# Optimization experiments

Measured on AMD Instinct MI355X. Metric: run time of the kernel, lower is better.

The kernel has to match this reference:

```python
import jax, jax.numpy as jnp
from jax import lax
import numpy as np

H = 512
W = 512
SIGMA = 0.1
IN_CH = [3, 66, 64, 64, 32, 32, 32, 16, 16]
OUT_CH = [64, 64, 64, 32, 32, 32, 16, 16, 16]
N_LAYERS = 9


def setup_inputs() -> dict:
    key = jax.random.key(0)
    ks = jax.random.split(key, 32)
    inp = {}
    inp['x'] = jax.random.uniform(ks[0], (3, 3, 1, 1), jnp.float32)  # query + 2 neighbor coords
    inp['neighbors'] = jax.random.uniform(ks[1], (2, 3, H, W), jnp.float32)
    inp['albedo_index'] = 4
    for i in range(N_LAYERS):
        kh = 1 if i == 0 else 3
        fan_in = IN_CH[i] * kh * kh
        inp[f'w{i}'] = jax.random.normal(ks[2 + i], (OUT_CH[i], IN_CH[i], kh, kh), jnp.float32) / np.sqrt(fan_in).astype(np.float32)
        inp[f'b{i}'] = jnp.zeros((OUT_CH[i],), jnp.float32)
    inp['wf'] = jax.random.normal(ks[20], (6, 16, 3, 3), jnp.float32) / np.sqrt(16 * 9).astype(np.float32)
    inp['bf'] = jnp.zeros((6,), jnp.float32)
    inp['albedos'] = 0.5 + jax.random.uniform(ks[21], (9, 3, H, W), jnp.float32)
    return inp


def _conv(x, w, b):
    y = lax.conv_general_dilated(x, w, (1, 1), 'VALID', dimension_numbers=('NCHW', 'OIHW', 'NCHW'))
    return y + b[None, :, None, None]


def _decoder(x, ws, bs, wf, bf):
    # coordconv constant [[ [0,2],[0,2] ], [ [0,0],[2,2] ]] with shape [2,2,2]
    coordconv = jnp.array([[[0., 2.], [0., 2.]], [[0., 0.], [2., 2.]]], dtype=x.dtype)
    for i in range(N_LAYERS):
        x = jnp.repeat(jnp.repeat(x, 2, axis=2), 2, axis=3)  # nearest upsample x2
        if i > 0:
            x = jnp.pad(x, ((0, 0), (0, 0), (1, 1), (1, 1)), mode='reflect')
        x = jax.nn.leaky_relu(_conv(x, ws[i], bs[i]), 0.01)
        if i == 0:
            cc = jnp.broadcast_to(coordconv[None], (x.shape[0],) + coordconv.shape)
            x = jnp.concatenate([x, cc], axis=1)  # -> 66 channels at 2x2
    x = jnp.pad(x, ((0, 0), (0, 0), (1, 1), (1, 1)), mode='reflect')
    return jnp.tanh(_conv(x, wf, bf))  # [B, 6, H, W]


def _grid_sample_border(img, grid):
    # bilinear, padding_mode='border', align_corners=False (matches torch grid_sample)
    N, C, Hh, Ww = img.shape
    gx = jnp.clip((grid[..., 0] + 1.0) * Ww / 2.0 - 0.5, 0.0, Ww - 1.0)
    gy = jnp.clip((grid[..., 1] + 1.0) * Hh / 2.0 - 0.5, 0.0, Hh - 1.0)
    x0 = jnp.floor(gx)
    y0 = jnp.floor(gy)
    wx = (gx - x0)[:, None]  # [N,1,H,W]
    wy = (gy - y0)[:, None]
    x0i = jnp.clip(x0.astype(jnp.int32), 0, Ww - 1)
    x1i = jnp.clip(x0i + 1, 0, Ww - 1)
    y0i = jnp.clip(y0.astype(jnp.int32), 0, Hh - 1)
    y1i = jnp.clip(y0i + 1, 0, Hh - 1)
    g = jax.vmap(lambda im, yi, xi: im[:, yi, xi])
    v00 = g(img, y0i, x0i)
    v01 = g(img, y0i, x1i)
    v10 = g(img, y1i, x0i)
    v11 = g(img, y1i, x1i)
    return v00 * (1 - wx) * (1 - wy) + v01 * wx * (1 - wy) + v10 * (1 - wx) * wy + v11 * wx * wy


def _blending(x, neighbors, flows, albedo):
    eps = 1e-5
    light_flow, view_flow, time_flow = flows[:1, 0:2], flows[:1, 2:4], flows[:1, 4:6]
    lf_n, vf_n, tf_n = flows[1:, 0:2], flows[1:, 2:4], flows[1:, 4:6]
    delta = x[:1] - x[1:]  # [2,3,1,1], broadcasts in place of torch.tile
    dl, dv, dt = delta[:, 0:1], delta[:, 1:2], delta[:, 2:3]
    flag = (jnp.abs(dl) > 0).astype(flows.dtype)
    offset_fwd = dl * light_flow + dv * view_flow + dt * time_flow  # [2,2,H,W]
    shading = flag * neighbors / albedo + (1 - flag) * neighbors
    ys = jnp.linspace(-1.0, 1.0, H)
    xs = jnp.linspace(-1.0, 1.0, W)
    grid_base = jnp.stack(jnp.meshgrid(xs, ys, indexing='xy'), axis=-1)  # [H,W,2], (...,0)=x
    grid = grid_base[None] + offset_fwd.transpose(0, 2, 3, 1)  # [2,H,W,2]
    warped_shading = _grid_sample_border(shading, grid)
    warped_vf = _grid_sample_border(vf_n, grid)
    warped_tf = _grid_sample_border(tf_n, grid)
    warped_lf = _grid_sample_border(lf_n, grid)
    warped_image = flag * warped_shading * albedo + (1 - flag) * warped_shading
    offset_bwd = dl * warped_lf + dv * warped_vf + dt * warped_tf
    dist = jnp.sum(jnp.abs(offset_fwd - offset_bwd), axis=1, keepdims=True)
    weight = jnp.exp(-SIGMA * W * dist)
    wn = weight / (jnp.sum(weight, axis=0, keepdims=True) + eps)
    return jnp.sum(warped_image * wn, axis=0, keepdims=True)  # [1,3,H,W]


def reference(x, neighbors, albedo_index, w0, w1, w2, w3, w4, w5, w6, w7, w8,
              b0, b1, b2, b3, b4, b5, b6, b7, b8, wf, bf, albedos):
    ws = [w0, w1, w2, w3, w4, w5, w6, w7, w8]
    bs = [b0, b1, b2, b3, b4, b5, b6, b7, b8]
    flows = _decoder(x, ws, bs, wf, bf)
    albedo = albedos[albedo_index]  # [3,H,W]
    return _blending(x, neighbors, flows, albedo)
```

## Files before the change

kernel.cpp:

```cpp
#include <hip/hip_runtime.h>
#include <hip/hip_bf16.h>
#include <math.h>


#define HH 512
#define WWI 512
#define HWP (HH*WWI)

__device__ __forceinline__ int xcd_swz(int bx, int nbx) {
  if ((nbx & 7) == 0) {
    int c = nbx >> 3;
    return (bx & 7) * c + (bx >> 3);
  }
  return bx;
}

__global__ void k_layer0(const float* __restrict__ xin, const float* __restrict__ w,
                         const float* __restrict__ bias, float* __restrict__ out)
{
  for (int idx = threadIdx.x; idx < 3*66*4; idx += blockDim.x) {
    int pos = idx & 3;
    int c = (idx >> 2) % 66;
    int b = idx / (66*4);
    float v;
    if (c < 64) {
      float a = bias[c];
      #pragma unroll
      for (int ci = 0; ci < 3; ci++) a += w[c*3+ci] * xin[b*3+ci];
      v = (a >= 0.f) ? a : 0.01f*a;
    } else {
      int xx = pos & 1, yy = pos >> 1;
      v = (c == 64) ? 2.f*(float)xx : 2.f*(float)yy;
    }
    out[idx] = v;
  }
}

__global__ void k_foldw8(const float* __restrict__ w1, const float* __restrict__ w2,
                         const float* __restrict__ w3, const float* __restrict__ w4,
                         const float* __restrict__ w5, const float* __restrict__ w6,
                         const float* __restrict__ w7, const float* __restrict__ w8,
                         float* __restrict__ f1, float* __restrict__ f2,
                         float* __restrict__ f3, float* __restrict__ f4,
                         float* __restrict__ f5, float* __restrict__ f6,
                         float* __restrict__ f7, float* __restrict__ f8)
{
  int idx = blockIdx.x*blockDim.x + threadIdx.x;
  const float* w; float* f; int n;
  if      (idx < 4224)  { w = w1; f = f1; n = idx; }
  else if (idx < 8320)  { w = w2; f = f2; n = idx - 4224; }
  else if (idx < 10368) { w = w3; f = f3; n = idx - 8320; }
  else if (idx < 11392) { w = w4; f = f4; n = idx - 10368; }
  else if (idx < 12416) { w = w5; f = f5; n = idx - 11392; }
  else if (idx < 12928) { w = w6; f = f6; n = idx - 12416; }
  else if (idx < 13184) { w = w7; f = f7; n = idx - 12928; }
  else if (idx < 13440) { w = w8; f = f8; n = idx - 13184; }
  else return;

  const float* ws = w + (size_t)n*9;
  float W[9];
  #pragma unroll
  for (int k = 0; k < 9; k++) W[k] = ws[k];

  float a[2][2][3];
  #pragma unroll
  for (int c = 0; c < 3; c++) {
    a[0][0][c] = W[c];          a[0][1][c] = W[3+c] + W[6+c];
    a[1][0][c] = W[c] + W[3+c]; a[1][1][c] = W[6+c];
  }
  float* fo = f + (size_t)n*16;
  #pragma unroll
  for (int py = 0; py < 2; py++)
    #pragma unroll
    for (int px = 0; px < 2; px++) {
      int p = py*2 + px;
      #pragma unroll
      for (int ky = 0; ky < 2; ky++) {
        float kx0 = (px == 0) ? a[py][ky][0] : (a[py][ky][0] + a[py][ky][1]);
        float kx1 = (px == 0) ? (a[py][ky][1] + a[py][ky][2]) : a[py][ky][2];
        fo[p*4 + ky*2 + 0] = kx0;
        fo[p*4 + ky*2 + 1] = kx1;
      }
    }
}

__global__ void k_upconv_s(const float* __restrict__ in, float* __restrict__ out,
                           const float* __restrict__ wfold, const float* __restrict__ bias,
                           int B, int Cin, int CO, int Hin)
{
  extern __shared__ float4 wlds4[];
  int nt = blockDim.x, tid = threadIdx.x;
  int co = blockIdx.y;
  int stride = Cin + 1;
  const float4* wsrc = reinterpret_cast<const float4*>(wfold);
  for (int s = tid; s < Cin*4; s += nt) {
    int p = s & 3;
    int ci = s >> 2;
    wlds4[p*stride + ci] = wsrc[(size_t)(co*Cin + ci)*4 + p];
  }
  __syncthreads();

  int Hout = Hin * 2;
  int npix = B * Hout * Hout;
  int idx = blockIdx.x*nt + tid;
  if (idx >= npix) return;
  int x = idx % Hout;
  int y = (idx / Hout) % Hout;
  int b = idx / (Hout * Hout);

  int X = x >> 1, Y = y >> 1;
  int px = x & 1, py = y & 1;

  int r_lo = py ? Y : (Y > 0 ? Y-1 : 0);
  int r_hi = py ? (Y < Hin-1 ? Y+1 : Hin-1) : Y;
  int c_lo = px ? X : (X > 0 ? X-1 : 0);
  int c_hi = px ? (X < Hin-1 ? X+1 : Hin-1) : X;

  float acc = bias[co];

  const size_t plane = (size_t)Hin * Hin;
  const float* ibase = in + (size_t)b * Cin * plane;
  const float4* wb = wlds4 + (py*2 + px) * stride;

  for (int ci = 0; ci < Cin; ci++) {
    const float* ip = ibase + (size_t)ci * plane;
    const float* rl = ip + (size_t)r_lo * Hin;
    const float* rh = ip + (size_t)r_hi * Hin;
    float4 w4 = wb[ci];
    acc += w4.x*rl[c_lo] + w4.y*rl[c_hi] + w4.z*rh[c_lo] + w4.w*rh[c_hi];
  }

  float v = (acc >= 0.f) ? acc : 0.01f*acc;
  out[((size_t)b*CO + co)*((size_t)Hout*Hout) + (size_t)y*Hout + x] = v;
}

template<int COB, int P>
__global__ void k_upconv_wP(const float* __restrict__ in, float* __restrict__ out,
                            const float* __restrict__ wfold, const float* __restrict__ bias,
                            int B, int Cin, int CO, int Hin)
{
  extern __shared__ float4 wlds4[];
  int nt = blockDim.x, tid = threadIdx.x;
  int co0 = blockIdx.y * COB;
  int stride = Cin * COB + 1;
  int nw = Cin * COB * 4;
  const float4* wsrc = reinterpret_cast<const float4*>(wfold);
  for (int s = tid; s < nw; s += nt) {
    int p = s & 3;
    int r = s >> 2;
    int ci = r % Cin;
    int col = r / Cin;
    wlds4[p*stride + ci*COB + col] = wsrc[(size_t)((co0 + col)*Cin + ci)*4 + p];
  }
  __syncthreads();

  int Hout = Hin * 2;
  int q = Hout / P;
  int total = B * Hout * q;
  int bx = xcd_swz(blockIdx.x, gridDim.x);
  int idx = bx*nt + tid;
  if (idx >= total) return;
  int x1 = idx % q;
  int y  = (idx / q) % Hout;
  int b  = idx / (q * Hout);

  int px = x1 & 1, py = y & 1;
  int Y = y >> 1;
  int r_lo = py ? Y : (Y > 0 ? Y-1 : 0);
  int r_hi = py ? (Y < Hin-1 ? Y+1 : Hin-1) : Y;

  int clo[P], chi[P];
  #pragma unroll
  for (int k = 0; k < P; k++) {
    int X = (x1 + k*q) >> 1;
    clo[k] = px ? X : (X > 0 ? X-1 : 0);
    chi[k] = px ? (X < Hin-1 ? X+1 : Hin-1) : X;
  }

  float acc[P][COB];
  #pragma unroll
  for (int j = 0; j < COB; j++) {
    float bv = bias[co0 + j];
    #pragma unroll
    for (int k = 0; k < P; k++) acc[k][j] = bv;
  }

  const size_t plane = (size_t)Hin * Hin;
  const float* ibase = in + (size_t)b * Cin * plane;
  const float4* wb = wlds4 + (py*2 + px) * stride;

  for (int ci = 0; ci < Cin; ci++) {
    const float* ip = ibase + (size_t)ci * plane;
    const float* rl = ip + (size_t)r_lo * Hin;
    const float* rh = ip + (size_t)r_hi * Hin;
    float pl0[P], pl1[P], ph0[P], ph1[P];
    #pragma unroll
    for (int k = 0; k < P; k++) {
      pl0[k] = rl[clo[k]]; pl1[k] = rl[chi[k]];
      ph0[k] = rh[clo[k]]; ph1[k] = rh[chi[k]];
    }
    const float4* wc = wb + ci * COB;
    #pragma unroll
    for (int j = 0; j < COB; j++) {
      float4 w4 = wc[j];
      #pragma unroll
      for (int k = 0; k < P; k++)
        acc[k][j] += w4.x*pl0[k] + w4.y*pl1[k] + w4.z*ph0[k] + w4.w*ph1[k];
    }
  }

  size_t oplane = (size_t)Hout * Hout;
  float* op = out + ((size_t)b * CO + co0) * oplane + (size_t)y*Hout + x1;
  #pragma unroll
  for (int j = 0; j < COB; j++) {
    #pragma unroll
    for (int k = 0; k < P; k++) {
      float v = acc[k][j];
      v = (v >= 0.f) ? v : 0.01f*v;
      op[k*q] = v;
    }
    op += oplane;
  }
}

__global__ void k_final2(const float* __restrict__ in, float* __restrict__ out,
                         const float* __restrict__ w, const float* __restrict__ bias)
{
  int total = 3 * HH * (WWI/2);
  int bx = xcd_swz(blockIdx.x, gridDim.x);
  int idx = bx*blockDim.x + threadIdx.x;
  if (idx >= total) return;
  int xh = idx % (WWI/2);
  int y  = (idx / (WWI/2)) % HH;
  int b  = idx / (HH * (WWI/2));
  int x0 = 2*xh;

  int ry[3];
  #pragma unroll
  for (int d = 0; d < 3; d++) {
    int t = y - 1 + d;
    t = (t < 0) ? -t : t;
    ry[d] = (t >= HH) ? (2*(HH-1) - t) : t;
  }
  int cx[4];
  cx[0] = (x0 == 0) ? 1 : x0-1;
  cx[1] = x0;
  cx[2] = x0+1;
  cx[3] = (x0+2 >= WWI) ? (2*(WWI-1) - (x0+2)) : x0+2;

  float acc0[6], acc1[6];
  #pragma unroll
  for (int co = 0; co < 6; co++) { float bv = bias[co]; acc0[co] = bv; acc1[co] = bv; }

  for (int ci = 0; ci < 16; ci++) {
    const float* ib = in + ((size_t)(b*16) + ci) * HWP;
    float p[3][4];
    #pragma unroll
    for (int dy = 0; dy < 3; dy++) {
      const float* r = ib + (size_t)ry[dy]*WWI;
      #pragma unroll
      for (int dx = 0; dx < 4; dx++) p[dy][dx] = r[cx[dx]];
    }
    const float* wc = w + ci*9;
    #pragma unroll
    for (int co = 0; co < 6; co++) {
      const float* wcc = wc + co*16*9;
      #pragma unroll
      for (int dy = 0; dy < 3; dy++) {
        #pragma unroll
        for (int dx = 0; dx < 3; dx++) {
          float wv = wcc[dy*3+dx];
          acc0[co] += wv * p[dy][dx];
          acc1[co] += wv * p[dy][dx+1];
        }
      }
    }
  }

  size_t pix = (size_t)y*WWI + x0;
  #pragma unroll
  for (int co = 0; co < 6; co++) {
    float2 v = make_float2(tanhf(acc0[co]), tanhf(acc1[co]));
    *reinterpret_cast<float2*>(out + ((size_t)(b*6) + co)*HWP + pix) = v;
  }
}

__global__ void k_blend(const float* __restrict__ xin, const float* __restrict__ neighbors,
                        const int* __restrict__ aidx, const float* __restrict__ albedos,
                        const float* __restrict__ flows, float* __restrict__ out)
{
  int idx = blockIdx.x*blockDim.x + threadIdx.x;
  if (idx >= HWP) return;
  int xo = idx & (WWI-1);
  int yo = idx >> 9;

  float xv[9];
  #pragma unroll
  for (int i = 0; i < 9; i++) xv[i] = xin[i];

  float f0[6];
  #pragma unroll
  for (int c = 0; c < 6; c++) f0[c] = flows[(size_t)c*HWP + idx];

  const float* alb = albedos + (size_t)aidx[0]*3*HWP;
  float albp[3];
  #pragma unroll
  for (int ch = 0; ch < 3; ch++) albp[ch] = alb[(size_t)ch*HWP + idx];

  float num0 = 0.f, num1 = 0.f, num2 = 0.f;
  float wsum = 0.f;

  #pragma unroll
  for (int n = 0; n < 2; n++) {
    float dl = xv[0] - xv[(n+1)*3 + 0];
    float dv = xv[1] - xv[(n+1)*3 + 1];
    float dt = xv[2] - xv[(n+1)*3 + 2];
    bool fl = fabsf(dl) > 0.f;

    float ofx = dl*f0[0] + dv*f0[2] + dt*f0[4];
    float ofy = dl*f0[1] + dv*f0[3] + dt*f0[5];

    float gx = ((-1.f + (2.f/511.f)*(float)xo) + ofx + 1.f)*256.f - 0.5f;
    float gy = ((-1.f + (2.f/511.f)*(float)yo) + ofy + 1.f)*256.f - 0.5f;
    gx = fminf(fmaxf(gx, 0.f), 511.f);
    gy = fminf(fmaxf(gy, 0.f), 511.f);

    float x0f = floorf(gx), y0f = floorf(gy);
    float wx = gx - x0f, wy = gy - y0f;
    int x0i = (int)x0f, y0i = (int)y0f;
    int x1i = min(x0i + 1, WWI-1), y1i = min(y0i + 1, HH-1);

    float cw[4] = {(1.f-wx)*(1.f-wy), wx*(1.f-wy), (1.f-wx)*wy, wx*wy};
    int   cp[4] = {y0i*WWI + x0i, y0i*WWI + x1i, y1i*WWI + x0i, y1i*WWI + x1i};

    const float* nb = neighbors + (size_t)n*3*HWP;
    const float* Fn = flows + (size_t)(n+1)*6*HWP;

    float s0=0.f,s1=0.f,s2=0.f;
    float l0=0.f,l1=0.f,v0=0.f,v1=0.f,t0=0.f,t1=0.f;
    #pragma unroll
    for (int c = 0; c < 4; c++) {
      int p = cp[c];
      float ww = cw[c];
      float n0 = nb[p];
      float n1 = nb[HWP + p];
      float n2 = nb[2*HWP + p];
      if (fl) {
        n0 /= alb[p];
        n1 /= alb[HWP + p];
        n2 /= alb[2*HWP + p];
      }
      s0 += ww*n0; s1 += ww*n1; s2 += ww*n2;
      l0 += ww*Fn[p];             l1 += ww*Fn[HWP + p];
      v0 += ww*Fn[2*HWP + p];     v1 += ww*Fn[3*HWP + p];
      t0 += ww*Fn[4*HWP + p];     t1 += ww*Fn[5*HWP + p];
    }

    float wi0 = fl ? s0*albp[0] : s0;
    float wi1 = fl ? s1*albp[1] : s1;
    float wi2 = fl ? s2*albp[2] : s2;

    float obx = dl*l0 + dv*v0 + dt*t0;
    float oby = dl*l1 + dv*v1 + dt*t1;
    float dist = fabsf(ofx - obx) + fabsf(ofy - oby);
    float wgt = expf(-51.2f * dist);

    wsum += wgt;
    num0 += wgt*wi0; num1 += wgt*wi1; num2 += wgt*wi2;
  }

  float inv = 1.f / (wsum + 1e-5f);
  out[idx]         = num0*inv;
  out[HWP + idx]   = num1*inv;
  out[2*HWP + idx] = num2*inv;
}

extern "C" void kernel_launch(void* const* d_in, const int* in_sizes, int n_in,
                              void* d_out, int out_size, void* d_ws, size_t ws_size,
                              hipStream_t stream) {
  const float* x         = (const float*)d_in[0];
  const float* neighbors = (const float*)d_in[1];
  const int*   aidx      = (const int*)d_in[2];
  const float* wts[10];
  const float* bis[10];
  for (int i = 0; i < 9; i++) { wts[i] = (const float*)d_in[3+2*i]; bis[i] = (const float*)d_in[4+2*i]; }
  wts[9] = (const float*)d_in[21];
  bis[9] = (const float*)d_in[22];
  const float* albedos = (const float*)d_in[23];

  float* wk   = (float*)d_ws;
  float* bufS = wk;
  float* bufA = wk + 800;
  float* bufB = bufA + 4718592;
  size_t need = (size_t)(800 + 4718592 + 12582912) * 4;
  if (ws_size < need) return;

  float* wf1 = bufA + 3200000;
  float* wf2 = wf1 + 67584;
  float* wf3 = wf2 + 65536;
  float* wf4 = wf3 + 32768;
  float* wf5 = wf4 + 16384;
  float* wf6 = wf5 + 16384;
  float* wf7 = wf6 + 8192;
  float* wf8 = wf7 + 4096;
  k_foldw8<<<53, 256, 0, stream>>>(wts[1], wts[2], wts[3], wts[4], wts[5], wts[6], wts[7], wts[8],
                                   wf1, wf2, wf3, wf4, wf5, wf6, wf7, wf8);

  k_layer0<<<1, 256, 0, stream>>>(x, wts[0], bis[0], bufS);

  auto blocks = [](int total){ return (total + 255) / 256; };

  {
    dim3 g1(blocks(3*4*4), 64), g2(blocks(3*8*8), 64);
    dim3 g3(blocks(3*16*16), 32), g4(blocks(3*32*32), 32), g5(blocks(3*64*64), 32);
    k_upconv_s<<<g1, 256, (size_t)4*(66+1)*16, stream>>>(bufS, bufA, wf1, bis[1], 3, 66, 64, 2);
    k_upconv_s<<<g2, 256, (size_t)4*(64+1)*16, stream>>>(bufA, bufB, wf2, bis[2], 3, 64, 64, 4);
    k_upconv_s<<<g3, 256, (size_t)4*(64+1)*16, stream>>>(bufB, bufA, wf3, bis[3], 3, 64, 32, 8);
    k_upconv_s<<<g4, 256, (size_t)4*(32+1)*16, stream>>>(bufA, bufB, wf4, bis[4], 3, 32, 32, 16);
    k_upconv_s<<<g5, 256, (size_t)4*(32+1)*16, stream>>>(bufB, bufA, wf5, bis[5], 3, 32, 32, 32);
  }

  {
    dim3 g6(blocks(3*128*32), 4);
    dim3 g7(blocks(3*256*64), 4);
    dim3 g8(blocks(3*512*128), 4);
    k_upconv_wP<4,4><<<g6, 256, (size_t)4*(32*4+1)*16, stream>>>(bufA, bufB, wf6, bis[6], 3, 32, 16, 64);
    k_upconv_wP<4,4><<<g7, 256, (size_t)4*(16*4+1)*16, stream>>>(bufB, bufA, wf7, bis[7], 3, 16, 16, 128);
    k_upconv_wP<4,4><<<g8, 256, (size_t)4*(16*4+1)*16, stream>>>(bufA, bufB, wf8, bis[8], 3, 16, 16, 256);
  }

  k_final2<<<blocks(3*HH*(WWI/2)), 256, 0, stream>>>(bufB, bufA, wts[9], bis[9]);
  k_blend<<<blocks(HWP), 256, 0, stream>>>(x, neighbors, aidx, albedos, bufA, (float*)d_out);
}
```

Baseline: 302.3 us.

## Fuse decoder layers 0-4 into one shared-memory head kernel

Replaces the layer-0 kernel and the four small upconv launches (layers 1-4) with a single kernel that keeps the intermediate activations in shared memory, one batch element per group of blocks, with the last layer's output channels split across 4 blocks. The goal is to remove four launch gaps and the global-memory round trips for these tiny layers. In exchange, layers 1-3 are recomputed redundantly in each of the 4 blocks per batch item and run on only 12 blocks, so those early layers have very little parallelism.

```diff
diff --git a/kernel.cpp b/kernel.cpp
--- a/kernel.cpp
+++ b/kernel.cpp
@@ -6,6 +6,7 @@
 #define HH 512
 #define WWI 512
 #define HWP (HH*WWI)
+#define PARTS 4
 
 __device__ __forceinline__ int xcd_swz(int bx, int nbx) {
   if ((nbx & 7) == 0) {
@@ -13,27 +14,6 @@
     return (bx & 7) * c + (bx >> 3);
   }
   return bx;
-}
-
-__global__ void k_layer0(const float* __restrict__ xin, const float* __restrict__ w,
-                         const float* __restrict__ bias, float* __restrict__ out)
-{
-  for (int idx = threadIdx.x; idx < 3*66*4; idx += blockDim.x) {
-    int pos = idx & 3;
-    int c = (idx >> 2) % 66;
-    int b = idx / (66*4);
-    float v;
-    if (c < 64) {
-      float a = bias[c];
-      #pragma unroll
-      for (int ci = 0; ci < 3; ci++) a += w[c*3+ci] * xin[b*3+ci];
-      v = (a >= 0.f) ? a : 0.01f*a;
-    } else {
-      int xx = pos & 1, yy = pos >> 1;
-      v = (c == 64) ? 2.f*(float)xx : 2.f*(float)yy;
-    }
-    out[idx] = v;
-  }
 }
 
 __global__ void k_foldw8(const float* __restrict__ w1, const float* __restrict__ w2,
@@ -84,6 +64,163 @@
     }
 }
 
+__global__ __launch_bounds__(1024)
+void k_head(const float* __restrict__ x, const float* __restrict__ w0,
+            const float* __restrict__ b0,
+            const float* __restrict__ wf1, const float* __restrict__ wf2,
+            const float* __restrict__ wf3, const float* __restrict__ wf4,
+            const float* __restrict__ b1, const float* __restrict__ b2,
+            const float* __restrict__ b3, const float* __restrict__ b4,
+            float* __restrict__ outL4)
+{
+  __shared__ float s_in[264];
+  __shared__ float s_l1[1024];
+  __shared__ float s_l2[4096];
+  __shared__ float s_l3[8192];
+
+  int t = threadIdx.x;
+  int bb   = blockIdx.x / PARTS;
+  int part = blockIdx.x % PARTS;
+
+  if (t < 264) {
+    int pos = t & 3;
+    int c = t >> 2;
+    float v;
+    if (c < 64) {
+      float a = b0[c];
+      #pragma unroll
+      for (int ci = 0; ci < 3; ci++) a += w0[c*3+ci] * x[bb*3+ci];
+      v = (a >= 0.f) ? a : 0.01f*a;
+    } else {
+      int xx = pos & 1, yy = pos >> 1;
+      v = (c == 64) ? 2.f*(float)xx : 2.f*(float)yy;
+    }
+    s_in[t] = v;
+  }
+  __syncthreads();
+
+  if (t < 256) {
+    int pix = t & 15, cog = t >> 4;
+    int y = pix >> 2, xx = pix & 3;
+    int X = xx >> 1, Y = y >> 1, px = xx & 1, py = y & 1;
+    int p = py*2 + px;
+    int r_lo = py ? Y : (Y > 0 ? Y-1 : 0);
+    int r_hi = py ? (Y < 1 ? Y+1 : 1) : Y;
+    int c_lo = px ? X : (X > 0 ? X-1 : 0);
+    int c_hi = px ? (X < 1 ? X+1 : 1) : X;
+    float acc[4];
+    #pragma unroll
+    for (int j = 0; j < 4; j++) acc[j] = b1[cog*4 + j];
+    for (int ci = 0; ci < 66; ci++) {
+      const float* ib = s_in + ci*4;
+      float p00 = ib[r_lo*2 + c_lo], p01 = ib[r_lo*2 + c_hi];
+      float p10 = ib[r_hi*2 + c_lo], p11 = ib[r_hi*2 + c_hi];
+      #pragma unroll
+      for (int j = 0; j < 4; j++) {
+        float4 w4 = *reinterpret_cast<const float4*>(wf1 + (size_t)((cog*4+j)*66 + ci)*16 + p*4);
+        acc[j] += w4.x*p00 + w4.y*p01 + w4.z*p10 + w4.w*p11;
+      }
+    }
+    #pragma unroll
+    for (int j = 0; j < 4; j++) {
+      float v = acc[j];
+      s_l1[(cog*4+j)*16 + pix] = (v >= 0.f) ? v : 0.01f*v;
+    }
+  }
+  __syncthreads();
+
+  if (t < 256) {
+    int pix = t & 63, cog = t >> 6;
+    int y = pix >> 3, xx = pix & 7;
+    int X = xx >> 1, Y = y >> 1, px = xx & 1, py = y & 1;
+    int p = py*2 + px;
+    int r_lo = py ? Y : (Y > 0 ? Y-1 : 0);
+    int r_hi = py ? (Y < 3 ? Y+1 : 3) : Y;
+    int c_lo = px ? X : (X > 0 ? X-1 : 0);
+    int c_hi = px ? (X < 3 ? X+1 : 3) : X;
+    float acc[16];
+    #pragma unroll
+    for (int j = 0; j < 16; j++) acc[j] = b2[cog*16 + j];
+    for (int ci = 0; ci < 64; ci++) {
+      const float* ib = s_l1 + ci*16;
+      float p00 = ib[r_lo*4 + c_lo], p01 = ib[r_lo*4 + c_hi];
+      float p10 = ib[r_hi*4 + c_lo], p11 = ib[r_hi*4 + c_hi];
+      #pragma unroll
+      for (int j = 0; j < 16; j++) {
+        float4 w4 = *reinterpret_cast<const float4*>(wf2 + (size_t)((cog*16+j)*64 + ci)*16 + p*4);
+        acc[j] += w4.x*p00 + w4.y*p01 + w4.z*p10 + w4.w*p11;
+      }
+    }
+    #pragma unroll
+    for (int j = 0; j < 16; j++) {
+      float v = acc[j];
+      s_l2[(cog*16+j)*64 + pix] = (v >= 0.f) ? v : 0.01f*v;
+    }
+  }
+  __syncthreads();
+
+  if (t < 512) {
+    int pix = t & 255, cog = t >> 8;
+    int y = pix >> 4, xx = pix & 15;
+    int X = xx >> 1, Y = y >> 1, px = xx & 1, py = y & 1;
+    int p = py*2 + px;
+    int r_lo = py ? Y : (Y > 0 ? Y-1 : 0);
+    int r_hi = py ? (Y < 7 ? Y+1 : 7) : Y;
+    int c_lo = px ? X : (X > 0 ? X-1 : 0);
+    int c_hi = px ? (X < 7 ? X+1 : 7) : X;
+    float acc[16];
+    #pragma unroll
+    for (int j = 0; j < 16; j++) acc[j] = b3[cog*16 + j];
+    for (int ci = 0; ci < 64; ci++) {
+      const float* ib = s_l2 + ci*64;
+      float p00 = ib[r_lo*8 + c_lo], p01 = ib[r_lo*8 + c_hi];
+      float p10 = ib[r_hi*8 + c_lo], p11 = ib[r_hi*8 + c_hi];
+      #pragma unroll
+      for (int j = 0; j < 16; j++) {
+        float4 w4 = *reinterpret_cast<const float4*>(wf3 + (size_t)((cog*16+j)*64 + ci)*16 + p*4);
+        acc[j] += w4.x*p00 + w4.y*p01 + w4.z*p10 + w4.w*p11;
+      }
+    }
+    #pragma unroll
+    for (int j = 0; j < 16; j++) {
+      float v = acc[j];
+      s_l3[(cog*16+j)*256 + pix] = (v >= 0.f) ? v : 0.01f*v;
+    }
+  }
+  __syncthreads();
+
+  {
+    int pix = t;
+    int y = pix >> 5, xx = pix & 31;
+    int X = xx >> 1, Y = y >> 1, px = xx & 1, py = y & 1;
+    int p = py*2 + px;
+    int r_lo = py ? Y : (Y > 0 ? Y-1 : 0);
+    int r_hi = py ? (Y < 15 ? Y+1 : 15) : Y;
+    int c_lo = px ? X : (X > 0 ? X-1 : 0);
+    int c_hi = px ? (X < 15 ? X+1 : 15) : X;
+    int co0 = part * 8;
+    float acc[8];
+    #pragma unroll
+    for (int j = 0; j < 8; j++) acc[j] = b4[co0 + j];
+    for (int ci = 0; ci < 32; ci++) {
+      const float* ib = s_l3 + ci*256;
+      float p00 = ib[r_lo*16 + c_lo], p01 = ib[r_lo*16 + c_hi];
+      float p10 = ib[r_hi*16 + c_lo], p11 = ib[r_hi*16 + c_hi];
+      #pragma unroll
+      for (int j = 0; j < 8; j++) {
+        float4 w4 = *reinterpret_cast<const float4*>(wf4 + (size_t)((co0+j)*32 + ci)*16 + p*4);
+        acc[j] += w4.x*p00 + w4.y*p01 + w4.z*p10 + w4.w*p11;
+      }
+    }
+    #pragma unroll
+    for (int j = 0; j < 8; j++) {
+      float v = acc[j];
+      v = (v >= 0.f) ? v : 0.01f*v;
+      outL4[((size_t)bb*32 + co0 + j)*1024 + pix] = v;
+    }
+  }
+}
+
 __global__ void k_upconv_s(const float* __restrict__ in, float* __restrict__ out,
                            const float* __restrict__ wfold, const float* __restrict__ bias,
                            int B, int Cin, int CO, int Hin)
@@ -394,6 +531,7 @@
   float* bufB = bufA + 4718592;
   size_t need = (size_t)(800 + 4718592 + 12582912) * 4;
   if (ws_size < need) return;
+  (void)bufS;
 
   float* wf1 = bufA + 3200000;
   float* wf2 = wf1 + 67584;
@@ -406,17 +544,13 @@
   k_foldw8<<<53, 256, 0, stream>>>(wts[1], wts[2], wts[3], wts[4], wts[5], wts[6], wts[7], wts[8],
                                    wf1, wf2, wf3, wf4, wf5, wf6, wf7, wf8);
 
-  k_layer0<<<1, 256, 0, stream>>>(x, wts[0], bis[0], bufS);
+  k_head<<<3*PARTS, 1024, 0, stream>>>(x, wts[0], bis[0], wf1, wf2, wf3, wf4,
+                                       bis[1], bis[2], bis[3], bis[4], bufB);
 
   auto blocks = [](int total){ return (total + 255) / 256; };
 
   {
-    dim3 g1(blocks(3*4*4), 64), g2(blocks(3*8*8), 64);
-    dim3 g3(blocks(3*16*16), 32), g4(blocks(3*32*32), 32), g5(blocks(3*64*64), 32);
-    k_upconv_s<<<g1, 256, (size_t)4*(66+1)*16, stream>>>(bufS, bufA, wf1, bis[1], 3, 66, 64, 2);
-    k_upconv_s<<<g2, 256, (size_t)4*(64+1)*16, stream>>>(bufA, bufB, wf2, bis[2], 3, 64, 64, 4);
-    k_upconv_s<<<g3, 256, (size_t)4*(64+1)*16, stream>>>(bufB, bufA, wf3, bis[3], 3, 64, 32, 8);
-    k_upconv_s<<<g4, 256, (size_t)4*(32+1)*16, stream>>>(bufA, bufB, wf4, bis[4], 3, 32, 32, 16);
+    dim3 g5(blocks(3*64*64), 32);
     k_upconv_s<<<g5, 256, (size_t)4*(32+1)*16, stream>>>(bufB, bufA, wf5, bis[5], 3, 32, 32, 32);
   }
 
```

After: 393.3 us. 1.3x slower.
